# Optimization experiments

Measured on AMD Instinct MI355X. Metric: run time of the kernel, lower is better.

## Reference

```python
import math
import jax, jax.numpy as jnp
from jax import lax
import numpy as np

D = 128            # head_dim
B = 16             # independent KV streams (e.g., heads)
S = 4096           # update sequence length
P = 4096           # reconstruction positions
MAX_SEQ_LEN = 8192
# (n_waves, ema_rate, freq_low, freq_high) per level, coarse -> fine
LEVELS = [(16, 0.001, 0.01, 1.0), (32, 0.005, 0.5, 3.0), (64, 0.02, 1.0, 6.0), (128, 0.05, 2.0, 10.0), (256, 0.1, 4.0, 20.0)]
TWO_PI = 2.0 * math.pi


def setup_inputs() -> dict:
    key = jax.random.key(0)
    ks = jax.random.split(key, 2 + len(LEVELS))
    inp = {}
    inp['kv_vectors'] = jax.random.normal(ks[0], (B, S, D), dtype=jnp.float32)
    inp['positions'] = jnp.arange(S, dtype=jnp.int32)
    inp['recon_positions'] = jnp.sort(jax.random.randint(ks[1], (P,), 0, MAX_SEQ_LEN, dtype=jnp.int32))
    for i, (n, a, lo, hi) in enumerate(LEVELS):
        k1, k2 = jax.random.split(ks[2 + i], 2)
        inp[f'W_enc_{i}'] = jax.random.normal(k1, (3 * n, D), dtype=jnp.float32) / math.sqrt(D)
        inp[f'W_dec_{i}'] = jax.random.normal(k2, (D, n), dtype=jnp.float32) / math.sqrt(n)
        inp[f'base_freqs_{i}'] = jnp.linspace(lo, hi, n, dtype=jnp.float32)
    return inp


def _ema_final(x, alpha):
    # x: [S, ...]; returns EMA state after S sequential steps from zero init.
    def step(c, xt):
        return (1.0 - alpha) * c + alpha * xt, None
    final, _ = lax.scan(step, jnp.zeros(x.shape[1:], x.dtype), x)
    return final


def _forward(kv_vectors, positions, recon_positions, params):
    pos_norm = positions.astype(jnp.float32)[:, None] / MAX_SEQ_LEN    # [S,1]
    rpos_norm = recon_positions.astype(jnp.float32)[:, None] / MAX_SEQ_LEN  # [P,1]
    out = jnp.zeros((kv_vectors.shape[0], recon_positions.shape[0], D), jnp.float32)
    for (n, alpha, _lo, _hi), (W_enc, W_dec, base_freqs) in zip(LEVELS, params):
        deltas = jnp.einsum('bsd,wd->bsw', kv_vectors, W_enc)          # [B,S,3n]
        d_freq, d_amp, d_phase = jnp.split(deltas, 3, axis=-1)         # each [B,S,n]
        pos_signal = jnp.sin(base_freqs[None, :] * pos_norm * TWO_PI)  # [S,n]
        xs = jnp.stack([d_freq * pos_signal[None], jnp.abs(d_amp), d_phase], axis=0)  # [3,B,S,n]
        xs = jnp.transpose(xs, (2, 0, 1, 3))                           # [S,3,B,n]
        freqs, amps, phases = _ema_final(xs, alpha)                    # each [B,n]
        wave_phases = TWO_PI * (freqs[:, None, :] + base_freqs[None, None, :]) * rpos_norm[None] + phases[:, None, :]
        wave_values = amps[:, None, :] * jnp.sin(wave_phases)          # [B,P,n]
        out = out + jnp.einsum('bpn,dn->bpd', wave_values, W_dec)
    return out


def reference(kv_vectors, positions, recon_positions,
              W_enc_0, W_dec_0, base_freqs_0,
              W_enc_1, W_dec_1, base_freqs_1,
              W_enc_2, W_dec_2, base_freqs_2,
              W_enc_3, W_dec_3, base_freqs_3,
              W_enc_4, W_dec_4, base_freqs_4):
    params = [(W_enc_0, W_dec_0, base_freqs_0), (W_enc_1, W_dec_1, base_freqs_1),
              (W_enc_2, W_dec_2, base_freqs_2), (W_enc_3, W_dec_3, base_freqs_3),
              (W_enc_4, W_dec_4, base_freqs_4)]
    return _forward(kv_vectors, positions, recon_positions, params)
```

## Files before the change

### kernel.cpp

```cpp
#include <hip/hip_runtime.h>

typedef __attribute__((ext_vector_type(8))) short short8;
typedef __attribute__((ext_vector_type(4))) float floatx4;

#define NLEV 5
#define B_   16
#define S_   4096
#define D_   128
#define P_   4096
#define CTOT 496
#define BP   (B_ * CTOT)
#define WPADG 512
#define CENC 1488
#define INV2PI 0.15915494309189535f
#define NJBLK 336

__device__ __forceinline__ unsigned short f2bf(float f) {
    unsigned u = __float_as_uint(f);
    u += 0x7fffu + ((u >> 16) & 1u);
    return (unsigned short)(u >> 16);
}
__device__ __forceinline__ unsigned int pack2(float a, float b) {
    return (unsigned int)f2bf(a) | ((unsigned int)f2bf(b) << 16);
}

__global__ void pack_weights(const float* __restrict__ we0, const float* __restrict__ we1,
                             const float* __restrict__ we2, const float* __restrict__ we3,
                             const float* __restrict__ we4,
                             const float* __restrict__ wd0, const float* __restrict__ wd1,
                             const float* __restrict__ wd2, const float* __restrict__ wd3,
                             const float* __restrict__ wd4,
                             unsigned short* __restrict__ wencb,
                             unsigned short* __restrict__ wdbT)
{
    int idx = blockIdx.x * 256 + threadIdx.x;
    const int NE = CENC * D_;
    if (idx < NE) {
        int c = idx >> 7, d = idx & 127;
        const float* src; int off;
        if (c < 48)        { src = we0; off = 0;   }
        else if (c < 144)  { src = we1; off = 48;  }
        else if (c < 336)  { src = we2; off = 144; }
        else               { src = (c < 720) ? we3 : we4; off = (c < 720) ? 336 : 720; }
        wencb[idx] = f2bf(src[(size_t)(c - off) * D_ + d]);
    } else {
        int k = idx - NE;
        if (k >= D_ * WPADG) return;
        int d = k >> 9, w = k & 511;
        float v = 0.0f;
        if (w < CTOT) {
            const float* src; int off, nl;
            if (w < 16)       { src = wd0; off = 0;   nl = 16;  }
            else if (w < 48)  { src = wd1; off = 16;  nl = 32;  }
            else if (w < 112) { src = wd2; off = 48;  nl = 64;  }
            else if (w < 240) { src = wd3; off = 112; nl = 128; }
            else              { src = wd4; off = 240; nl = 256; }
            v = src[(size_t)d * nl + (w - off)];
        }
        wdbT[k] = f2bf(v);
    }
}

__global__ __launch_bounds__(256) void encoder(
    const float* __restrict__ kv, const int* __restrict__ positions,
    const unsigned short* __restrict__ wencb,
    const float* __restrict__ bfr0, const float* __restrict__ bfr1,
    const float* __restrict__ bfr2, const float* __restrict__ bfr3,
    const float* __restrict__ bfr4,
    float* __restrict__ accb)
{
    __shared__ unsigned short kvb[64 * 136];
    __shared__ float pf[64];
    const int b   = blockIdx.y;
    const int bid = blockIdx.x;
    const int tid = threadIdx.x;

    int bx, lb;
    if (bid < 96)       { bx = bid / 24;            lb = bid % 24; }
    else if (bid < 144) { int r = bid - 96;  bx = 4 + r / 12; lb = r % 12; }
    else if (bid < 192) { int r = bid - 144; bx = 8 + r / 6;  lb = r % 6;  }
    else                { int r = bid - 192; bx = 16 + r / 3; lb = r % 3;  }
    const int t0 = S_ - 64 * (bx + 1);

    const float* src = kv + ((size_t)(b * S_ + t0)) * D_;
    #pragma unroll
    for (int f = 0; f < 8; ++f) {
        int idx = f * 256 + tid;
        int t = idx >> 5, d4 = idx & 31;
        float4 val = *(const float4*)(src + t * D_ + d4 * 4);
        unsigned long long u = (unsigned long long)pack2(val.x, val.y)
                             | ((unsigned long long)pack2(val.z, val.w) << 32);
        *(unsigned long long*)&kvb[t * 136 + d4 * 4] = u;
    }
    if (tid < 64) pf[tid] = (float)positions[t0 + tid] * (1.0f / 8192.0f);
    __syncthreads();

    const int wid = tid >> 6, lane = tid & 63, ln = lane & 15, quad = lane >> 4;

    const int cnt = 9 + (bx < 16 ? 12 : 0) + (bx < 8 ? 24 : 0) + (bx < 4 ? 48 : 0);
    int jid = lb * 4 + wid;
    if (jid >= cnt) return;

    const int   n_l[5]  = {16, 32, 64, 128, 256};
    const int   coff[5] = {0, 16, 48, 112, 240};
    const int   c3[5]   = {0, 48, 144, 336, 720};
    const float al[5]   = {0.001f, 0.005f, 0.02f, 0.05f, 0.1f};
    const float l2m[5]  = {-0.0014434169f, -0.0072315692f, -0.0291463449f,
                           -0.0740005794f, -0.1520030934f};
    const float* bfp[5] = {bfr0, bfr1, bfr2, bfr3, bfr4};

    int l = 0, ci = jid;
    {
        const int sz[5] = {3, 6, (bx < 16 ? 12 : 0), (bx < 8 ? 24 : 0), (bx < 4 ? 48 : 0)};
        #pragma unroll
        for (int q = 0; q < 4; ++q) {
            if (ci >= sz[l]) { ci -= sz[l]; ++l; }
        }
    }
    const int n = n_l[l];

    const unsigned short* wrow = wencb + (size_t)(c3[l] + ci * 16 + ln) * D_;
    floatx4 acc[4];
    #pragma unroll
    for (int m = 0; m < 4; ++m) acc[m] = (floatx4){0.f, 0.f, 0.f, 0.f};
    #pragma unroll
    for (int k = 0; k < 4; ++k) {
        short8 bfg = *(const short8*)(wrow + k * 32 + quad * 8);
        #pragma unroll
        for (int m = 0; m < 4; ++m) {
            short8 af = *(const short8*)&kvb[(m * 16 + ln) * 136 + k * 32 + quad * 8];
            acc[m] = __builtin_amdgcn_mfma_f32_16x16x32_bf16(af, bfg, acc[m], 0, 0, 0);
        }
    }

    const int kind  = (ci * 16) / n;
    const int local = ci * 16 + ln - kind * n;
    const float bsv = (kind == 0) ? bfp[l][local] : 0.0f;
    float s = 0.0f;
    #pragma unroll
    for (int m = 0; m < 4; ++m)
        #pragma unroll
        for (int r = 0; r < 4; ++r) {
            int   trel = m * 16 + quad * 4 + r;
            int   tg   = t0 + trel;
            float wt   = al[l] * exp2f((float)(S_ - 1 - tg) * l2m[l]);
            float v    = acc[m][r];
            if (kind == 0) {
                float rev = bsv * pf[trel];
                rev -= floorf(rev);
                v *= __builtin_amdgcn_sinf(rev);
            } else if (kind == 1) {
                v = fabsf(v);
            }
            s += wt * v;
        }
    s += __shfl_xor(s, 16);
    s += __shfl_xor(s, 32);
    if (lane < 16)
        atomicAdd(accb + (size_t)kind * BP + b * CTOT + coff[l] + local, s);
}

__global__ void combine(const float* __restrict__ accb,
                        float* __restrict__ parA, float* __restrict__ parQ,
                        float* __restrict__ parP,
                        const float* __restrict__ b0, const float* __restrict__ b1,
                        const float* __restrict__ b2, const float* __restrict__ b3,
                        const float* __restrict__ b4)
{
    int idx = blockIdx.x * 256 + threadIdx.x;
    if (idx >= B_ * WPADG) return;
    int b = idx >> 9, w = idx & 511;
    float A = 0.f, Q = 0.f, P = 0.f;
    if (w < CTOT) {
        const float* bf; int off;
        if (w < 16)       { bf = b0; off = 0;   }
        else if (w < 48)  { bf = b1; off = 16;  }
        else if (w < 112) { bf = b2; off = 48;  }
        else if (w < 240) { bf = b3; off = 112; }
        else              { bf = b4; off = 240; }
        float f  = accb[0 * BP + b * CTOT + w];
        A        = accb[1 * BP + b * CTOT + w];
        float ph = accb[2 * BP + b * CTOT + w];
        Q = f + bf[w - off];
        P = ph * INV2PI;
    }
    parA[idx] = A; parQ[idx] = Q; parP[idx] = P;
}

__global__ __launch_bounds__(256) void decoder(
    const float* __restrict__ parA, const float* __restrict__ parQ,
    const float* __restrict__ parP,
    const unsigned short* __restrict__ wdbT, const int* __restrict__ rpos,
    float* __restrict__ out)
{
    __shared__ unsigned short v[64 * 264];
    __shared__ float rpn[64];
    const int b = blockIdx.y, p0 = blockIdx.x * 64, tid = threadIdx.x;
    if (tid < 64) rpn[tid] = (float)rpos[p0 + tid] * (1.0f / 8192.0f);

    const int wid = tid >> 6, lane = tid & 63, ln = lane & 15, quad = lane >> 4;
    const int nt0 = wid * 2;

    floatx4 acc[4][2];
    #pragma unroll
    for (int m = 0; m < 4; ++m)
        #pragma unroll
        for (int j = 0; j < 2; ++j) acc[m][j] = (floatx4){0.f, 0.f, 0.f, 0.f};

    #pragma unroll
    for (int half = 0; half < 2; ++half) {
        const int w0 = half * 256;
        float Q  = parQ[b * WPADG + w0 + tid];
        float A  = parA[b * WPADG + w0 + tid];
        float Ph = parP[b * WPADG + w0 + tid];
        __syncthreads();
        for (int p = 0; p < 64; ++p) {
            float r = fmaf(Q, rpn[p], Ph);
            r -= floorf(r);
            v[p * 264 + tid] = f2bf(A * __builtin_amdgcn_sinf(r));
        }
        __syncthreads();

        #pragma unroll
        for (int kk = 0; kk < 8; ++kk) {
            short8 bn[2];
            #pragma unroll
            for (int j = 0; j < 2; ++j)
                bn[j] = *(const short8*)(wdbT + (size_t)((nt0 + j) * 16 + ln) * WPADG
                                         + w0 + kk * 32 + quad * 8);
            short8 am[4];
            #pragma unroll
            for (int m = 0; m < 4; ++m)
                am[m] = *(const short8*)&v[(m * 16 + ln) * 264 + kk * 32 + quad * 8];
            #pragma unroll
            for (int m = 0; m < 4; ++m)
                #pragma unroll
                for (int j = 0; j < 2; ++j)
                    acc[m][j] = __builtin_amdgcn_mfma_f32_16x16x32_bf16(
                                    am[m], bn[j], acc[m][j], 0, 0, 0);
        }
    }

    #pragma unroll
    for (int m = 0; m < 4; ++m)
        #pragma unroll
        for (int j = 0; j < 2; ++j)
            #pragma unroll
            for (int r = 0; r < 4; ++r) {
                int p = p0 + m * 16 + quad * 4 + r;
                int d = (nt0 + j) * 16 + ln;
                out[((size_t)(b * P_ + p)) * D_ + d] = acc[m][j][r];
            }
}

extern "C" void kernel_launch(void* const* d_in, const int* in_sizes, int n_in,
                              void* d_out, int out_size, void* d_ws, size_t ws_size,
                              hipStream_t stream)
{
    const float* kv        = (const float*)d_in[0];
    const int*   positions = (const int*)d_in[1];
    const int*   rpos      = (const int*)d_in[2];

    char* ws = (char*)d_ws;
    float*          accb  = (float*)(ws + 0);
    float*          parA  = (float*)(ws + 95232);
    float*          parQ  = (float*)(ws + 128000);
    float*          parP  = (float*)(ws + 160768);
    unsigned short* wencb = (unsigned short*)(ws + 193536);
    unsigned short* wdbT  = (unsigned short*)(ws + 574464);

    hipMemsetAsync(accb, 0, (size_t)(3 * BP) * sizeof(float), stream);

    pack_weights<<<1000, 256, 0, stream>>>(
        (const float*)d_in[3], (const float*)d_in[6], (const float*)d_in[9],
        (const float*)d_in[12], (const float*)d_in[15],
        (const float*)d_in[4], (const float*)d_in[7], (const float*)d_in[10],
        (const float*)d_in[13], (const float*)d_in[16],
        wencb, wdbT);

    encoder<<<dim3(NJBLK, B_), 256, 0, stream>>>(
        kv, positions, wencb,
        (const float*)d_in[5], (const float*)d_in[8], (const float*)d_in[11],
        (const float*)d_in[14], (const float*)d_in[17],
        accb);

    combine<<<(B_ * WPADG) / 256, 256, 0, stream>>>(
        accb, parA, parQ, parP,
        (const float*)d_in[5], (const float*)d_in[8], (const float*)d_in[11],
        (const float*)d_in[14], (const float*)d_in[17]);

    decoder<<<dim3(P_ / 64, B_), 256, 0, stream>>>(
        parA, parQ, parP, wdbT, rpos, (float*)d_out);
}
```

Before: 161.7 us.

## Pre-convert KV to bf16, load encoder fragments from registers, fuse combine into decoder

A single pack kernel now converts the whole KV tensor to bf16, packs the weights and zeroes the accumulator, which replaces the separate memset launch. The encoder drops its shared-memory staging. Each wave loads its A fragments straight from global into registers and loops over several channel chunks, so fewer workgroups (72 per stream) reuse the same KV tile. The combine kernel is folded into the decoder's prologue, removing one launch and the intermediate parameter arrays. In exchange, the bf16 copy of KV costs an extra global write and read, and the encoder has less parallelism.

```diff
diff --git a/kernel.cpp b/kernel.cpp
--- a/kernel.cpp
+++ b/kernel.cpp
@@ -3,7 +3,6 @@
 typedef __attribute__((ext_vector_type(8))) short short8;
 typedef __attribute__((ext_vector_type(4))) float floatx4;
 
-#define NLEV 5
 #define B_   16
 #define S_   4096
 #define D_   128
@@ -13,7 +12,6 @@
 #define WPADG 512
 #define CENC 1488
 #define INV2PI 0.15915494309189535f
-#define NJBLK 336
 
 __device__ __forceinline__ unsigned short f2bf(float f) {
     unsigned u = __float_as_uint(f);
@@ -24,82 +22,100 @@
     return (unsigned int)f2bf(a) | ((unsigned int)f2bf(b) << 16);
 }
 
-__global__ void pack_weights(const float* __restrict__ we0, const float* __restrict__ we1,
-                             const float* __restrict__ we2, const float* __restrict__ we3,
-                             const float* __restrict__ we4,
-                             const float* __restrict__ wd0, const float* __restrict__ wd1,
-                             const float* __restrict__ wd2, const float* __restrict__ wd3,
-                             const float* __restrict__ wd4,
-                             unsigned short* __restrict__ wencb,
-                             unsigned short* __restrict__ wdbT)
+#define NKVB 4096
+#define NWB  1000
+#define NZB  93
+__global__ void pack_all(const float* __restrict__ kv,
+                         const float* __restrict__ we0, const float* __restrict__ we1,
+                         const float* __restrict__ we2, const float* __restrict__ we3,
+                         const float* __restrict__ we4,
+                         const float* __restrict__ wd0, const float* __restrict__ wd1,
+                         const float* __restrict__ wd2, const float* __restrict__ wd3,
+                         const float* __restrict__ wd4,
+                         unsigned short* __restrict__ kvb16,
+                         unsigned short* __restrict__ wencb,
+                         unsigned short* __restrict__ wdbT,
+                         float* __restrict__ accb)
 {
-    int idx = blockIdx.x * 256 + threadIdx.x;
-    const int NE = CENC * D_;
-    if (idx < NE) {
-        int c = idx >> 7, d = idx & 127;
-        const float* src; int off;
-        if (c < 48)        { src = we0; off = 0;   }
-        else if (c < 144)  { src = we1; off = 48;  }
-        else if (c < 336)  { src = we2; off = 144; }
-        else               { src = (c < 720) ? we3 : we4; off = (c < 720) ? 336 : 720; }
-        wencb[idx] = f2bf(src[(size_t)(c - off) * D_ + d]);
+    const int bid = blockIdx.x, tid = threadIdx.x;
+    if (bid < NKVB) {
+        size_t base = ((size_t)bid * 256 + tid) * 8;
+        float4 a = *(const float4*)(kv + base);
+        float4 c = *(const float4*)(kv + base + 4);
+        union { unsigned int u[4]; short8 s; } r;
+        r.u[0] = pack2(a.x, a.y); r.u[1] = pack2(a.z, a.w);
+        r.u[2] = pack2(c.x, c.y); r.u[3] = pack2(c.z, c.w);
+        *(short8*)(kvb16 + base) = r.s;
+    } else if (bid < NKVB + NWB) {
+        int idx = (bid - NKVB) * 256 + tid;
+        const int NE = CENC * D_;
+        if (idx < NE) {
+            int c = idx >> 7, d = idx & 127;
+            const float* src; int off;
+            if (c < 48)        { src = we0; off = 0;   }
+            else if (c < 144)  { src = we1; off = 48;  }
+            else if (c < 336)  { src = we2; off = 144; }
+            else               { src = (c < 720) ? we3 : we4; off = (c < 720) ? 336 : 720; }
+            wencb[idx] = f2bf(src[(size_t)(c - off) * D_ + d]);
+        } else {
+            int k = idx - NE;
+            int d = k >> 9, w = k & 511;
+            float v = 0.0f;
+            if (w < CTOT) {
+                const float* src; int off, nl;
+                if (w < 16)       { src = wd0; off = 0;   nl = 16;  }
+                else if (w < 48)  { src = wd1; off = 16;  nl = 32;  }
+                else if (w < 112) { src = wd2; off = 48;  nl = 64;  }
+                else if (w < 240) { src = wd3; off = 112; nl = 128; }
+                else              { src = wd4; off = 240; nl = 256; }
+                v = src[(size_t)d * nl + (w - off)];
+            }
+            wdbT[k] = f2bf(v);
+        }
     } else {
-        int k = idx - NE;
-        if (k >= D_ * WPADG) return;
-        int d = k >> 9, w = k & 511;
-        float v = 0.0f;
-        if (w < CTOT) {
-            const float* src; int off, nl;
-            if (w < 16)       { src = wd0; off = 0;   nl = 16;  }
-            else if (w < 48)  { src = wd1; off = 16;  nl = 32;  }
-            else if (w < 112) { src = wd2; off = 48;  nl = 64;  }
-            else if (w < 240) { src = wd3; off = 112; nl = 128; }
-            else              { src = wd4; off = 240; nl = 256; }
-            v = src[(size_t)d * nl + (w - off)];
-        }
-        wdbT[k] = f2bf(v);
+        int idx = (bid - NKVB - NWB) * 256 + tid;
+        if (idx < 3 * BP) accb[idx] = 0.0f;
     }
 }
 
 __global__ __launch_bounds__(256) void encoder(
-    const float* __restrict__ kv, const int* __restrict__ positions,
+    const unsigned short* __restrict__ kvb16, const int* __restrict__ positions,
     const unsigned short* __restrict__ wencb,
     const float* __restrict__ bfr0, const float* __restrict__ bfr1,
     const float* __restrict__ bfr2, const float* __restrict__ bfr3,
     const float* __restrict__ bfr4,
     float* __restrict__ accb)
 {
-    __shared__ unsigned short kvb[64 * 136];
-    __shared__ float pf[64];
-    const int b   = blockIdx.y;
-    const int bid = blockIdx.x;
-    const int tid = threadIdx.x;
-
-    int bx, lb;
-    if (bid < 96)       { bx = bid / 24;            lb = bid % 24; }
-    else if (bid < 144) { int r = bid - 96;  bx = 4 + r / 12; lb = r % 12; }
-    else if (bid < 192) { int r = bid - 144; bx = 8 + r / 6;  lb = r % 6;  }
-    else                { int r = bid - 192; bx = 16 + r / 3; lb = r % 3;  }
-    const int t0 = S_ - 64 * (bx + 1);
-
-    const float* src = kv + ((size_t)(b * S_ + t0)) * D_;
-    #pragma unroll
-    for (int f = 0; f < 8; ++f) {
-        int idx = f * 256 + tid;
-        int t = idx >> 5, d4 = idx & 31;
-        float4 val = *(const float4*)(src + t * D_ + d4 * 4);
-        unsigned long long u = (unsigned long long)pack2(val.x, val.y)
-                             | ((unsigned long long)pack2(val.z, val.w) << 32);
-        *(unsigned long long*)&kvb[t * 136 + d4 * 4] = u;
-    }
-    if (tid < 64) pf[tid] = (float)positions[t0 + tid] * (1.0f / 8192.0f);
-    __syncthreads();
-
-    const int wid = tid >> 6, lane = tid & 63, ln = lane & 15, quad = lane >> 4;
-
-    const int cnt = 9 + (bx < 16 ? 12 : 0) + (bx < 8 ? 24 : 0) + (bx < 4 ? 48 : 0);
-    int jid = lb * 4 + wid;
-    if (jid >= cnt) return;
+    const int b    = blockIdx.y;
+    const int gw   = blockIdx.x * 4 + (threadIdx.x >> 6);
+    const int lane = threadIdx.x & 63, ln15 = lane & 15, quad = lane >> 4;
+
+    int bx, widx, nw;
+    if (gw < 96)       { bx = gw / 24;                widx = gw % 24;      nw = 24; }
+    else if (gw < 144) { int r = gw - 96;  bx = 4 + r / 12;  widx = r % 12; nw = 12; }
+    else if (gw < 192) { int r = gw - 144; bx = 8 + r / 6;   widx = r % 6;  nw = 6;  }
+    else               { int r = gw - 192; bx = 16 + r / 2;  widx = r % 2;  nw = 2;  }
+    const int t0  = S_ - 64 * (bx + 1);
+    const int sz2 = (bx < 16) ? 12 : 0, sz3 = (bx < 8) ? 24 : 0;
+    const int cnt = 9 + sz2 + sz3 + ((bx < 4) ? 48 : 0);
+
+    const unsigned short* abase = kvb16 + ((size_t)(b * S_ + t0 + ln15)) * D_ + quad * 8;
+    short8 afr[4][4];
+    #pragma unroll
+    for (int m = 0; m < 4; ++m)
+        #pragma unroll
+        for (int k = 0; k < 4; ++k)
+            afr[m][k] = *(const short8*)(abase + (m * 16) * D_ + k * 32);
+
+    float pfr[16];
+    #pragma unroll
+    for (int m = 0; m < 4; ++m) {
+        int4 pi = *(const int4*)(positions + t0 + m * 16 + quad * 4);
+        pfr[m * 4 + 0] = (float)pi.x * (1.0f / 8192.0f);
+        pfr[m * 4 + 1] = (float)pi.y * (1.0f / 8192.0f);
+        pfr[m * 4 + 2] = (float)pi.z * (1.0f / 8192.0f);
+        pfr[m * 4 + 3] = (float)pi.w * (1.0f / 8192.0f);
+    }
 
     const int   n_l[5]  = {16, 32, 64, 128, 256};
     const int   coff[5] = {0, 16, 48, 112, 240};
@@ -109,87 +125,69 @@
                            -0.0740005794f, -0.1520030934f};
     const float* bfp[5] = {bfr0, bfr1, bfr2, bfr3, bfr4};
 
-    int l = 0, ci = jid;
-    {
-        const int sz[5] = {3, 6, (bx < 16 ? 12 : 0), (bx < 8 ? 24 : 0), (bx < 4 ? 48 : 0)};
-        #pragma unroll
-        for (int q = 0; q < 4; ++q) {
-            if (ci >= sz[l]) { ci -= sz[l]; ++l; }
-        }
-    }
-    const int n = n_l[l];
-
-    const unsigned short* wrow = wencb + (size_t)(c3[l] + ci * 16 + ln) * D_;
-    floatx4 acc[4];
-    #pragma unroll
-    for (int m = 0; m < 4; ++m) acc[m] = (floatx4){0.f, 0.f, 0.f, 0.f};
-    #pragma unroll
-    for (int k = 0; k < 4; ++k) {
-        short8 bfg = *(const short8*)(wrow + k * 32 + quad * 8);
-        #pragma unroll
-        for (int m = 0; m < 4; ++m) {
-            short8 af = *(const short8*)&kvb[(m * 16 + ln) * 136 + k * 32 + quad * 8];
-            acc[m] = __builtin_amdgcn_mfma_f32_16x16x32_bf16(af, bfg, acc[m], 0, 0, 0);
-        }
-    }
-
-    const int kind  = (ci * 16) / n;
-    const int local = ci * 16 + ln - kind * n;
-    const float bsv = (kind == 0) ? bfp[l][local] : 0.0f;
-    float s = 0.0f;
-    #pragma unroll
-    for (int m = 0; m < 4; ++m)
-        #pragma unroll
-        for (int r = 0; r < 4; ++r) {
-            int   trel = m * 16 + quad * 4 + r;
-            int   tg   = t0 + trel;
-            float wt   = al[l] * exp2f((float)(S_ - 1 - tg) * l2m[l]);
-            float v    = acc[m][r];
-            if (kind == 0) {
-                float rev = bsv * pf[trel];
-                rev -= floorf(rev);
-                v *= __builtin_amdgcn_sinf(rev);
-            } else if (kind == 1) {
-                v = fabsf(v);
+    int   lprev = -1;
+    float wtr[16];
+
+    for (int ch = widx; ch < cnt; ch += nw) {
+        int c = ch, l = 0;
+        if (c >= 3) { c -= 3; l = 1;
+            if (c >= 6) { c -= 6; l = 2;
+                if (c >= sz2) { c -= sz2; l = 3;
+                    if (c >= sz3) { c -= sz3; l = 4; } } } }
+        const int ci = c, n = n_l[l];
+
+        if (l != lprev) {
+            lprev = l;
+            const float s1 = (float)(S_ - 1 - t0);
+            #pragma unroll
+            for (int i = 0; i < 16; ++i) {
+                float trel = (float)((i >> 2) * 16 + quad * 4 + (i & 3));
+                wtr[i] = al[l] * exp2f((s1 - trel) * l2m[l]);
             }
-            s += wt * v;
-        }
-    s += __shfl_xor(s, 16);
-    s += __shfl_xor(s, 32);
-    if (lane < 16)
-        atomicAdd(accb + (size_t)kind * BP + b * CTOT + coff[l] + local, s);
-}
-
-__global__ void combine(const float* __restrict__ accb,
-                        float* __restrict__ parA, float* __restrict__ parQ,
-                        float* __restrict__ parP,
-                        const float* __restrict__ b0, const float* __restrict__ b1,
-                        const float* __restrict__ b2, const float* __restrict__ b3,
-                        const float* __restrict__ b4)
-{
-    int idx = blockIdx.x * 256 + threadIdx.x;
-    if (idx >= B_ * WPADG) return;
-    int b = idx >> 9, w = idx & 511;
-    float A = 0.f, Q = 0.f, P = 0.f;
-    if (w < CTOT) {
-        const float* bf; int off;
-        if (w < 16)       { bf = b0; off = 0;   }
-        else if (w < 48)  { bf = b1; off = 16;  }
-        else if (w < 112) { bf = b2; off = 48;  }
-        else if (w < 240) { bf = b3; off = 112; }
-        else              { bf = b4; off = 240; }
-        float f  = accb[0 * BP + b * CTOT + w];
-        A        = accb[1 * BP + b * CTOT + w];
-        float ph = accb[2 * BP + b * CTOT + w];
-        Q = f + bf[w - off];
-        P = ph * INV2PI;
-    }
-    parA[idx] = A; parQ[idx] = Q; parP[idx] = P;
+        }
+
+        const unsigned short* wrow = wencb + (size_t)(c3[l] + ci * 16 + ln15) * D_ + quad * 8;
+        floatx4 acc[4];
+        #pragma unroll
+        for (int m = 0; m < 4; ++m) acc[m] = (floatx4){0.f, 0.f, 0.f, 0.f};
+        #pragma unroll
+        for (int k = 0; k < 4; ++k) {
+            short8 bfg = *(const short8*)(wrow + k * 32);
+            #pragma unroll
+            for (int m = 0; m < 4; ++m)
+                acc[m] = __builtin_amdgcn_mfma_f32_16x16x32_bf16(afr[m][k], bfg, acc[m], 0, 0, 0);
+        }
+
+        const int kind  = (ci * 16) / n;
+        const int local = ci * 16 + ln15 - kind * n;
+        const float bsv = (kind == 0) ? bfp[l][local] : 0.0f;
+        float s = 0.0f;
+        #pragma unroll
+        for (int m = 0; m < 4; ++m)
+            #pragma unroll
+            for (int r = 0; r < 4; ++r) {
+                float v = acc[m][r];
+                if (kind == 0) {
+                    float rev = bsv * pfr[m * 4 + r];
+                    rev -= floorf(rev);
+                    v *= __builtin_amdgcn_sinf(rev);
+                } else if (kind == 1) {
+                    v = fabsf(v);
+                }
+                s += wtr[m * 4 + r] * v;
+            }
+        s += __shfl_xor(s, 16);
+        s += __shfl_xor(s, 32);
+        if (lane < 16)
+            atomicAdd(accb + (size_t)kind * BP + b * CTOT + coff[l] + local, s);
+    }
 }
 
 __global__ __launch_bounds__(256) void decoder(
-    const float* __restrict__ parA, const float* __restrict__ parQ,
-    const float* __restrict__ parP,
+    const float* __restrict__ accb,
+    const float* __restrict__ b0, const float* __restrict__ b1,
+    const float* __restrict__ b2, const float* __restrict__ b3,
+    const float* __restrict__ b4,
     const unsigned short* __restrict__ wdbT, const int* __restrict__ rpos,
     float* __restrict__ out)
 {
@@ -198,6 +196,27 @@
     const int b = blockIdx.y, p0 = blockIdx.x * 64, tid = threadIdx.x;
     if (tid < 64) rpn[tid] = (float)rpos[p0 + tid] * (1.0f / 8192.0f);
 
+    float Qv[2], Av[2], Pv[2];
+    #pragma unroll
+    for (int h = 0; h < 2; ++h) {
+        int w = h * 256 + tid;
+        float A = 0.f, Q = 0.f, P = 0.f;
+        if (w < CTOT) {
+            const float* bf; int off;
+            if (w < 16)       { bf = b0; off = 0;   }
+            else if (w < 48)  { bf = b1; off = 16;  }
+            else if (w < 112) { bf = b2; off = 48;  }
+            else if (w < 240) { bf = b3; off = 112; }
+            else              { bf = b4; off = 240; }
+            float f  = accb[0 * BP + b * CTOT + w];
+            A        = accb[1 * BP + b * CTOT + w];
+            float ph = accb[2 * BP + b * CTOT + w];
+            Q = f + bf[w - off];
+            P = ph * INV2PI;
+        }
+        Qv[h] = Q; Av[h] = A; Pv[h] = P;
+    }
+
     const int wid = tid >> 6, lane = tid & 63, ln = lane & 15, quad = lane >> 4;
     const int nt0 = wid * 2;
 
@@ -210,9 +229,7 @@
     #pragma unroll
     for (int half = 0; half < 2; ++half) {
         const int w0 = half * 256;
-        float Q  = parQ[b * WPADG + w0 + tid];
-        float A  = parA[b * WPADG + w0 + tid];
-        float Ph = parP[b * WPADG + w0 + tid];
+        const float Q = Qv[half], A = Av[half], Ph = Pv[half];
         __syncthreads();
         for (int p = 0; p < 64; ++p) {
             float r = fmaf(Q, rpn[p], Ph);
@@ -263,32 +280,27 @@
 
     char* ws = (char*)d_ws;
     float*          accb  = (float*)(ws + 0);
-    float*          parA  = (float*)(ws + 95232);
-    float*          parQ  = (float*)(ws + 128000);
-    float*          parP  = (float*)(ws + 160768);
-    unsigned short* wencb = (unsigned short*)(ws + 193536);
-    unsigned short* wdbT  = (unsigned short*)(ws + 574464);
-
-    hipMemsetAsync(accb, 0, (size_t)(3 * BP) * sizeof(float), stream);
-
-    pack_weights<<<1000, 256, 0, stream>>>(
+    unsigned short* wencb = (unsigned short*)(ws + 95232);
+    unsigned short* wdbT  = (unsigned short*)(ws + 476160);
+    unsigned short* kvb16 = (unsigned short*)(ws + 607232);
+
+    pack_all<<<NKVB + NWB + NZB, 256, 0, stream>>>(
+        kv,
         (const float*)d_in[3], (const float*)d_in[6], (const float*)d_in[9],
         (const float*)d_in[12], (const float*)d_in[15],
         (const float*)d_in[4], (const float*)d_in[7], (const float*)d_in[10],
         (const float*)d_in[13], (const float*)d_in[16],
-        wencb, wdbT);
-
-    encoder<<<dim3(NJBLK, B_), 256, 0, stream>>>(
-        kv, positions, wencb,
+        kvb16, wencb, wdbT, accb);
+
+    encoder<<<dim3(72, B_), 256, 0, stream>>>(
+        kvb16, positions, wencb,
         (const float*)d_in[5], (const float*)d_in[8], (const float*)d_in[11],
         (const float*)d_in[14], (const float*)d_in[17],
         accb);
 
-    combine<<<(B_ * WPADG) / 256, 256, 0, stream>>>(
-        accb, parA, parQ, parP,
+    decoder<<<dim3(P_ / 64, B_), 256, 0, stream>>>(
+        accb,
         (const float*)d_in[5], (const float*)d_in[8], (const float*)d_in[11],
-        (const float*)d_in[14], (const float*)d_in[17]);
-
-    decoder<<<dim3(P_ / 64, B_), 256, 0, stream>>>(
-        parA, parQ, parP, wdbT, rpos, (float*)d_out);
-}
+        (const float*)d_in[14], (const float*)d_in[17],
+        wdbT, rpos, (float*)d_out);
+}
```

Measured after the change: 173.5 us. +7.3%, slower.
